# Kernel tuning notes

Measured on AMD Instinct MI355X. Metric: run time of the kernel, lower is better.

The kernel has to match this reference:

```python
import jax, jax.numpy as jnp
import numpy as np

M_FAI = 1024


def _cmul_mm(a, b):
    # complex matmul of (2, M, M) @ (2, M, M) -> (2, M, M)
    re = a[0] @ b[0] - a[1] @ b[1]
    im = a[0] @ b[1] + a[1] @ b[0]
    return jnp.stack([re, im])


def _cmul_el(a, b):
    # elementwise complex multiply, leading dim 2 = (real, imag)
    re = a[0] * b[0] - a[1] * b[1]
    im = a[0] * b[1] + a[1] * b[0]
    return jnp.stack([re, im])


def _diag(x):
    # diagonal of (2, M, M) -> (2, M)
    return jnp.diagonal(x, axis1=1, axis2=2)


def setup_inputs() -> dict:
    key = jax.random.key(0)
    ks = jax.random.split(key, 13)
    mats = {}
    names = ['Theta', 'A1', 'B1', 'C1', 'A2', 'B2', 'C2', 'A3', 'B3', 'C3']
    for i, n in enumerate(names):
        mats[n] = jax.random.normal(ks[i], (2, M_FAI, M_FAI), dtype=jnp.float32)
    mats['alpha'] = jnp.ones((1,), dtype=jnp.float32)
    mats['belta'] = jnp.ones((1,), dtype=jnp.float32)
    # xavier_uniform with gain=0.01 on (2, M_fai): bound = 0.01*sqrt(6/(2+M_fai))
    bound = 0.01 * np.sqrt(6.0 / (2 + M_FAI))
    mats['param1'] = jax.random.uniform(ks[10], (2, M_FAI), dtype=jnp.float32, minval=-bound, maxval=bound)
    mats['param2'] = jax.random.uniform(ks[11], (2, M_FAI), dtype=jnp.float32, minval=-bound, maxval=bound)
    return mats


def reference(Theta, A1, B1, C1, A2, B2, C2, A3, B3, C3, alpha, belta, param1, param2):
    # approximateTheta = cdiag(param1); diag(p) @ C == columnwise complex scale of C rows
    p = param1[:, :, None]  # (2, M, 1)
    Q1 = _cmul_mm(A1, _cmul_el(p, C1))
    Q2 = _cmul_mm(A2, _cmul_el(p, C2))
    Q3 = _cmul_mm(A2, _cmul_el(p, C3))  # original uses A2 here (faithful)

    Thd = _diag(Theta)  # (2, M)
    b1 = alpha * _cmul_el(_diag(A1), _cmul_el(Thd, _diag(C1))) - _diag(Q1) + _diag(B1)
    b2 = belta * _cmul_el(_diag(A2), _cmul_el(Thd, _diag(C2))) - _diag(Q2) + _diag(B2)
    b3 = belta * _cmul_el(_diag(A3), _cmul_el(Thd, _diag(C3))) - _diag(Q3) + _diag(B3)
    b = b1 + b2 + b3 + param2  # (2, M)
    # per-column complex unit-normalize: torch.norm over the (2,1) column
    norm = jnp.sqrt(jnp.sum(b * b, axis=0, keepdims=True))
    theta_new = b / norm  # (2, M)
    # cdiag: embed as (2, M, M) diagonal complex matrix
    Theta_new = jax.vmap(jnp.diag)(theta_new)
    return Theta_new
```

## Files before the change

kernel.cpp:

```cpp
#include <hip/hip_runtime.h>
#include <math.h>

#define M 1024

#define TI 32
#define KCH 32
#define KSPLIT 16
#define KB (M / KSPLIT)

__global__ __launch_bounds__(256)
void diagq_kernel(const float* __restrict__ A1, const float* __restrict__ C1,
                  const float* __restrict__ A2, const float* __restrict__ C2,
                  const float* __restrict__ C3, const float* __restrict__ p1,
                  float* __restrict__ D )
{
    __shared__ float As_re[TI][KCH + 1];
    __shared__ float As_im[TI][KCH + 1];
    __shared__ float Cs_re[KCH][TI];
    __shared__ float Cs_im[KCH][TI];
    __shared__ float red_re[256];
    __shared__ float red_im[256];

    const int t  = threadIdx.x;
    const int i0 = blockIdx.x * TI;
    const int q  = blockIdx.y;
    const int z  = blockIdx.z;
    const int k0 = z * KB;

    const float* __restrict__ A = (q == 0) ? A1 : A2;
    const float* __restrict__ C = (q == 0) ? C1 : ((q == 1) ? C2 : C3);

    const size_t MM = (size_t)M * M;

    const int l_row = t >> 3;
    const int l_c4  = (t & 7) << 2;

    const int i_local = t & 31;
    const int kslice  = t >> 5;

    float acc_re = 0.f, acc_im = 0.f;

    #pragma unroll
    for (int s = 0; s < KB / KCH; ++s) {
        const int kbase = k0 + s * KCH;

        {
            const size_t off = (size_t)(i0 + l_row) * M + kbase + l_c4;
            const float4 are = *(const float4*)(A + off);
            const float4 aim = *(const float4*)(A + MM + off);
            As_re[l_row][l_c4 + 0] = are.x; As_re[l_row][l_c4 + 1] = are.y;
            As_re[l_row][l_c4 + 2] = are.z; As_re[l_row][l_c4 + 3] = are.w;
            As_im[l_row][l_c4 + 0] = aim.x; As_im[l_row][l_c4 + 1] = aim.y;
            As_im[l_row][l_c4 + 2] = aim.z; As_im[l_row][l_c4 + 3] = aim.w;
        }
        {
            const int k = kbase + l_row;
            const float pre = p1[k];
            const float pim = p1[M + k];
            const size_t off = (size_t)k * M + i0 + l_c4;
            const float4 cre = *(const float4*)(C + off);
            const float4 cim = *(const float4*)(C + MM + off);
            Cs_re[l_row][l_c4 + 0] = pre * cre.x - pim * cim.x;
            Cs_re[l_row][l_c4 + 1] = pre * cre.y - pim * cim.y;
            Cs_re[l_row][l_c4 + 2] = pre * cre.z - pim * cim.z;
            Cs_re[l_row][l_c4 + 3] = pre * cre.w - pim * cim.w;
            Cs_im[l_row][l_c4 + 0] = pre * cim.x + pim * cre.x;
            Cs_im[l_row][l_c4 + 1] = pre * cim.y + pim * cre.y;
            Cs_im[l_row][l_c4 + 2] = pre * cim.z + pim * cre.z;
            Cs_im[l_row][l_c4 + 3] = pre * cim.w + pim * cre.w;
        }
        __syncthreads();

        #pragma unroll
        for (int j = 0; j < 4; ++j) {
            const int kk = (kslice << 2) + j;
            const float a_re = As_re[i_local][kk];
            const float a_im = As_im[i_local][kk];
            const float c_re = Cs_re[kk][i_local];
            const float c_im = Cs_im[kk][i_local];
            acc_re += a_re * c_re - a_im * c_im;
            acc_im += a_re * c_im + a_im * c_re;
        }
        __syncthreads();
    }

    red_re[t] = acc_re;
    red_im[t] = acc_im;
    __syncthreads();
    if (t < TI) {
        float sr = 0.f, si = 0.f;
        #pragma unroll
        for (int s = 0; s < 8; ++s) { sr += red_re[t + 32 * s]; si += red_im[t + 32 * s]; }
        D[((size_t)(q * 2 + 0) * KSPLIT + z) * M + i0 + t] = sr;
        D[((size_t)(q * 2 + 1) * KSPLIT + z) * M + i0 + t] = si;
    }
}

__global__ __launch_bounds__(256)
void finalize_kernel(const float* __restrict__ Theta,
                     const float* __restrict__ A1, const float* __restrict__ B1, const float* __restrict__ C1,
                     const float* __restrict__ A2, const float* __restrict__ B2, const float* __restrict__ C2,
                     const float* __restrict__ A3, const float* __restrict__ B3, const float* __restrict__ C3,
                     const float* __restrict__ alpha, const float* __restrict__ belta,
                     const float* __restrict__ p2, const float* __restrict__ D,
                     float* __restrict__ out)
{
    __shared__ float sv[128];

    const int t = threadIdx.x;
    const int i = blockIdx.x;
    const size_t MM = (size_t)M * M;
    const size_t dg = (size_t)i * M + i;

    if (t < 96) {
        sv[t] = D[(size_t)t * M + i];
    } else if (t < 116) {
        const int j = t - 96;
        const float* ptrs[10] = {Theta, A1, B1, C1, A2, B2, C2, A3, B3, C3};
        const float* P = ptrs[j >> 1];
        sv[t] = P[(j & 1) ? (MM + dg) : dg];
    } else if (t == 116) { sv[116] = p2[i]; }
    else if (t == 117)   { sv[117] = p2[M + i]; }
    else if (t == 118)   { sv[118] = alpha[0]; }
    else if (t == 119)   { sv[119] = belta[0]; }

    const float4 z4 = make_float4(0.f, 0.f, 0.f, 0.f);
    ((float4*)(out + (size_t)i * M))[t]      = z4;
    ((float4*)(out + MM + (size_t)i * M))[t] = z4;

    __syncthreads();

    if (t == 0) {
        float qs[6];
        #pragma unroll
        for (int qc = 0; qc < 6; ++qc) {
            float s = 0.f;
            #pragma unroll
            for (int k = 0; k < 16; ++k) s += sv[qc * 16 + k];
            qs[qc] = s;
        }
        const float th_re = sv[96], th_im = sv[97];
        const float al = sv[118], be = sv[119];

        float b_re = sv[116], b_im = sv[117];

        {
            const float a_re = sv[98],  a_im = sv[99];
            const float c_re = sv[102], c_im = sv[103];
            const float t_re = th_re * c_re - th_im * c_im;
            const float t_im = th_re * c_im + th_im * c_re;
            b_re += al * (a_re * t_re - a_im * t_im) - qs[0] + sv[100];
            b_im += al * (a_re * t_im + a_im * t_re) - qs[1] + sv[101];
        }
        {
            const float a_re = sv[104], a_im = sv[105];
            const float c_re = sv[108], c_im = sv[109];
            const float t_re = th_re * c_re - th_im * c_im;
            const float t_im = th_re * c_im + th_im * c_re;
            b_re += be * (a_re * t_re - a_im * t_im) - qs[2] + sv[106];
            b_im += be * (a_re * t_im + a_im * t_re) - qs[3] + sv[107];
        }
        {
            const float a_re = sv[110], a_im = sv[111];
            const float c_re = sv[114], c_im = sv[115];
            const float t_re = th_re * c_re - th_im * c_im;
            const float t_im = th_re * c_im + th_im * c_re;
            b_re += be * (a_re * t_re - a_im * t_im) - qs[4] + sv[112];
            b_im += be * (a_re * t_im + a_im * t_re) - qs[5] + sv[113];
        }

        const float inv = 1.0f / sqrtf(b_re * b_re + b_im * b_im);
        out[dg]      = b_re * inv;
        out[MM + dg] = b_im * inv;
    }
}

extern "C" void kernel_launch(void* const* d_in, const int* in_sizes, int n_in,
                              void* d_out, int out_size, void* d_ws, size_t ws_size,
                              hipStream_t stream) {
    const float* Theta = (const float*)d_in[0];
    const float* A1    = (const float*)d_in[1];
    const float* B1    = (const float*)d_in[2];
    const float* C1    = (const float*)d_in[3];
    const float* A2    = (const float*)d_in[4];
    const float* B2    = (const float*)d_in[5];
    const float* C2    = (const float*)d_in[6];
    const float* A3    = (const float*)d_in[7];
    const float* B3    = (const float*)d_in[8];
    const float* C3    = (const float*)d_in[9];
    const float* alpha = (const float*)d_in[10];
    const float* belta = (const float*)d_in[11];
    const float* p1    = (const float*)d_in[12];
    const float* p2    = (const float*)d_in[13];
    float* out = (float*)d_out;
    float* D   = (float*)d_ws;

    dim3 grid(M / TI, 3, KSPLIT);
    diagq_kernel<<<grid, 256, 0, stream>>>(A1, C1, A2, C2, C3, p1, D);

    finalize_kernel<<<dim3(M), 256, 0, stream>>>(
        Theta, A1, B1, C1, A2, B2, C2, A3, B3, C3, alpha, belta, p2, D, out);
}
```

Baseline: 130.5 us.

## Share A2 tile across Q2/Q3, move output zeroing into diag kernel, thin finalize

The diagonal-Q kernel now runs two block sets instead of three. The second set loads each A2 tile once and accumulates against both C2 and C3, which removes one redundant read pass over A2. Zero-filling the 8 MB output moves from the finalize kernel into the diag kernel, with each block clearing a slice. The finalize kernel becomes one thread per diagonal element and reads its inputs directly, with no shared staging or sync. In exchange, qset blocks carry more shared memory and branch work, and this relies on the zeroing finishing before finalize writes the diagonal, which stream ordering guarantees.

```diff
diff --git a/kernel.cpp b/kernel.cpp
--- a/kernel.cpp
+++ b/kernel.cpp
@@ -12,23 +12,33 @@
 void diagq_kernel(const float* __restrict__ A1, const float* __restrict__ C1,
                   const float* __restrict__ A2, const float* __restrict__ C2,
                   const float* __restrict__ C3, const float* __restrict__ p1,
-                  float* __restrict__ D )
+                  float* __restrict__ D ,
+                  float* __restrict__ out )
 {
     __shared__ float As_re[TI][KCH + 1];
     __shared__ float As_im[TI][KCH + 1];
-    __shared__ float Cs_re[KCH][TI];
-    __shared__ float Cs_im[KCH][TI];
-    __shared__ float red_re[256];
-    __shared__ float red_im[256];
-
-    const int t  = threadIdx.x;
-    const int i0 = blockIdx.x * TI;
-    const int q  = blockIdx.y;
-    const int z  = blockIdx.z;
-    const int k0 = z * KB;
-
-    const float* __restrict__ A = (q == 0) ? A1 : A2;
-    const float* __restrict__ C = (q == 0) ? C1 : ((q == 1) ? C2 : C3);
+    __shared__ float Cb_re[KCH][TI + 1];
+    __shared__ float Cb_im[KCH][TI + 1];
+    __shared__ float Cc_re[KCH][TI + 1];
+    __shared__ float Cc_im[KCH][TI + 1];
+    __shared__ float red[4][256];
+
+    const int t    = threadIdx.x;
+    const int i0   = blockIdx.x * TI;
+    const int qset = blockIdx.y;
+    const int z    = blockIdx.z;
+    const int k0   = z * KB;
+
+    {
+        const int bid = blockIdx.x + 32 * (blockIdx.y + 2 * blockIdx.z);
+        float4* o4 = (float4*)out + (size_t)bid * 512 + t;
+        const float4 z4 = make_float4(0.f, 0.f, 0.f, 0.f);
+        o4[0]   = z4;
+        o4[256] = z4;
+    }
+
+    const float* __restrict__ A  = qset ? A2 : A1;
+    const float* __restrict__ Cb = qset ? C2 : C1;
 
     const size_t MM = (size_t)M * M;
 
@@ -38,7 +48,8 @@
     const int i_local = t & 31;
     const int kslice  = t >> 5;
 
-    float acc_re = 0.f, acc_im = 0.f;
+    float b_re = 0.f, b_im = 0.f;
+    float c_re_acc = 0.f, c_im_acc = 0.f;
 
     #pragma unroll
     for (int s = 0; s < KB / KCH; ++s) {
@@ -53,21 +64,34 @@
             As_im[l_row][l_c4 + 0] = aim.x; As_im[l_row][l_c4 + 1] = aim.y;
             As_im[l_row][l_c4 + 2] = aim.z; As_im[l_row][l_c4 + 3] = aim.w;
         }
+        const int k = kbase + l_row;
+        const float pre = p1[k];
+        const float pim = p1[M + k];
         {
-            const int k = kbase + l_row;
-            const float pre = p1[k];
-            const float pim = p1[M + k];
             const size_t off = (size_t)k * M + i0 + l_c4;
-            const float4 cre = *(const float4*)(C + off);
-            const float4 cim = *(const float4*)(C + MM + off);
-            Cs_re[l_row][l_c4 + 0] = pre * cre.x - pim * cim.x;
-            Cs_re[l_row][l_c4 + 1] = pre * cre.y - pim * cim.y;
-            Cs_re[l_row][l_c4 + 2] = pre * cre.z - pim * cim.z;
-            Cs_re[l_row][l_c4 + 3] = pre * cre.w - pim * cim.w;
-            Cs_im[l_row][l_c4 + 0] = pre * cim.x + pim * cre.x;
-            Cs_im[l_row][l_c4 + 1] = pre * cim.y + pim * cre.y;
-            Cs_im[l_row][l_c4 + 2] = pre * cim.z + pim * cre.z;
-            Cs_im[l_row][l_c4 + 3] = pre * cim.w + pim * cre.w;
+            const float4 cre = *(const float4*)(Cb + off);
+            const float4 cim = *(const float4*)(Cb + MM + off);
+            Cb_re[l_row][l_c4 + 0] = pre * cre.x - pim * cim.x;
+            Cb_re[l_row][l_c4 + 1] = pre * cre.y - pim * cim.y;
+            Cb_re[l_row][l_c4 + 2] = pre * cre.z - pim * cim.z;
+            Cb_re[l_row][l_c4 + 3] = pre * cre.w - pim * cim.w;
+            Cb_im[l_row][l_c4 + 0] = pre * cim.x + pim * cre.x;
+            Cb_im[l_row][l_c4 + 1] = pre * cim.y + pim * cre.y;
+            Cb_im[l_row][l_c4 + 2] = pre * cim.z + pim * cre.z;
+            Cb_im[l_row][l_c4 + 3] = pre * cim.w + pim * cre.w;
+        }
+        if (qset) {
+            const size_t off = (size_t)k * M + i0 + l_c4;
+            const float4 cre = *(const float4*)(C3 + off);
+            const float4 cim = *(const float4*)(C3 + MM + off);
+            Cc_re[l_row][l_c4 + 0] = pre * cre.x - pim * cim.x;
+            Cc_re[l_row][l_c4 + 1] = pre * cre.y - pim * cim.y;
+            Cc_re[l_row][l_c4 + 2] = pre * cre.z - pim * cim.z;
+            Cc_re[l_row][l_c4 + 3] = pre * cre.w - pim * cim.w;
+            Cc_im[l_row][l_c4 + 0] = pre * cim.x + pim * cre.x;
+            Cc_im[l_row][l_c4 + 1] = pre * cim.y + pim * cre.y;
+            Cc_im[l_row][l_c4 + 2] = pre * cim.z + pim * cre.z;
+            Cc_im[l_row][l_c4 + 3] = pre * cim.w + pim * cre.w;
         }
         __syncthreads();
 
@@ -76,27 +100,49 @@
             const int kk = (kslice << 2) + j;
             const float a_re = As_re[i_local][kk];
             const float a_im = As_im[i_local][kk];
-            const float c_re = Cs_re[kk][i_local];
-            const float c_im = Cs_im[kk][i_local];
-            acc_re += a_re * c_re - a_im * c_im;
-            acc_im += a_re * c_im + a_im * c_re;
+            {
+                const float x_re = Cb_re[kk][i_local];
+                const float x_im = Cb_im[kk][i_local];
+                b_re += a_re * x_re - a_im * x_im;
+                b_im += a_re * x_im + a_im * x_re;
+            }
+            if (qset) {
+                const float x_re = Cc_re[kk][i_local];
+                const float x_im = Cc_im[kk][i_local];
+                c_re_acc += a_re * x_re - a_im * x_im;
+                c_im_acc += a_re * x_im + a_im * x_re;
+            }
         }
         __syncthreads();
     }
 
-    red_re[t] = acc_re;
-    red_im[t] = acc_im;
+    red[0][t] = b_re;
+    red[1][t] = b_im;
+    red[2][t] = c_re_acc;
+    red[3][t] = c_im_acc;
     __syncthreads();
     if (t < TI) {
-        float sr = 0.f, si = 0.f;
+        float s0 = 0.f, s1 = 0.f, s2 = 0.f, s3 = 0.f;
         #pragma unroll
-        for (int s = 0; s < 8; ++s) { sr += red_re[t + 32 * s]; si += red_im[t + 32 * s]; }
-        D[((size_t)(q * 2 + 0) * KSPLIT + z) * M + i0 + t] = sr;
-        D[((size_t)(q * 2 + 1) * KSPLIT + z) * M + i0 + t] = si;
+        for (int s = 0; s < 8; ++s) {
+            s0 += red[0][t + 32 * s];
+            s1 += red[1][t + 32 * s];
+            s2 += red[2][t + 32 * s];
+            s3 += red[3][t + 32 * s];
+        }
+        if (qset == 0) {
+            D[((size_t)(0 * KSPLIT) + z) * M + i0 + t] = s0;
+            D[((size_t)(1 * KSPLIT) + z) * M + i0 + t] = s1;
+        } else {
+            D[((size_t)(2 * KSPLIT) + z) * M + i0 + t] = s0;
+            D[((size_t)(3 * KSPLIT) + z) * M + i0 + t] = s1;
+            D[((size_t)(4 * KSPLIT) + z) * M + i0 + t] = s2;
+            D[((size_t)(5 * KSPLIT) + z) * M + i0 + t] = s3;
+        }
     }
 }
 
-__global__ __launch_bounds__(256)
+__global__ __launch_bounds__(128)
 void finalize_kernel(const float* __restrict__ Theta,
                      const float* __restrict__ A1, const float* __restrict__ B1, const float* __restrict__ C1,
                      const float* __restrict__ A2, const float* __restrict__ B2, const float* __restrict__ C2,
@@ -105,74 +151,53 @@
                      const float* __restrict__ p2, const float* __restrict__ D,
                      float* __restrict__ out)
 {
-    __shared__ float sv[128];
-
-    const int t = threadIdx.x;
-    const int i = blockIdx.x;
+    const int i = blockIdx.x * 128 + threadIdx.x;
     const size_t MM = (size_t)M * M;
     const size_t dg = (size_t)i * M + i;
 
-    if (t < 96) {
-        sv[t] = D[(size_t)t * M + i];
-    } else if (t < 116) {
-        const int j = t - 96;
-        const float* ptrs[10] = {Theta, A1, B1, C1, A2, B2, C2, A3, B3, C3};
-        const float* P = ptrs[j >> 1];
-        sv[t] = P[(j & 1) ? (MM + dg) : dg];
-    } else if (t == 116) { sv[116] = p2[i]; }
-    else if (t == 117)   { sv[117] = p2[M + i]; }
-    else if (t == 118)   { sv[118] = alpha[0]; }
-    else if (t == 119)   { sv[119] = belta[0]; }
-
-    const float4 z4 = make_float4(0.f, 0.f, 0.f, 0.f);
-    ((float4*)(out + (size_t)i * M))[t]      = z4;
-    ((float4*)(out + MM + (size_t)i * M))[t] = z4;
-
-    __syncthreads();
-
-    if (t == 0) {
-        float qs[6];
+    float qs[6];
+    #pragma unroll
+    for (int qc = 0; qc < 6; ++qc) {
+        float s = 0.f;
         #pragma unroll
-        for (int qc = 0; qc < 6; ++qc) {
-            float s = 0.f;
-            #pragma unroll
-            for (int k = 0; k < 16; ++k) s += sv[qc * 16 + k];
-            qs[qc] = s;
-        }
-        const float th_re = sv[96], th_im = sv[97];
-        const float al = sv[118], be = sv[119];
-
-        float b_re = sv[116], b_im = sv[117];
-
-        {
-            const float a_re = sv[98],  a_im = sv[99];
-            const float c_re = sv[102], c_im = sv[103];
-            const float t_re = th_re * c_re - th_im * c_im;
-            const float t_im = th_re * c_im + th_im * c_re;
-            b_re += al * (a_re * t_re - a_im * t_im) - qs[0] + sv[100];
-            b_im += al * (a_re * t_im + a_im * t_re) - qs[1] + sv[101];
-        }
-        {
-            const float a_re = sv[104], a_im = sv[105];
-            const float c_re = sv[108], c_im = sv[109];
-            const float t_re = th_re * c_re - th_im * c_im;
-            const float t_im = th_re * c_im + th_im * c_re;
-            b_re += be * (a_re * t_re - a_im * t_im) - qs[2] + sv[106];
-            b_im += be * (a_re * t_im + a_im * t_re) - qs[3] + sv[107];
-        }
-        {
-            const float a_re = sv[110], a_im = sv[111];
-            const float c_re = sv[114], c_im = sv[115];
-            const float t_re = th_re * c_re - th_im * c_im;
-            const float t_im = th_re * c_im + th_im * c_re;
-            b_re += be * (a_re * t_re - a_im * t_im) - qs[4] + sv[112];
-            b_im += be * (a_re * t_im + a_im * t_re) - qs[5] + sv[113];
-        }
-
-        const float inv = 1.0f / sqrtf(b_re * b_re + b_im * b_im);
-        out[dg]      = b_re * inv;
-        out[MM + dg] = b_im * inv;
-    }
+        for (int z = 0; z < KSPLIT; ++z)
+            s += D[((size_t)qc * KSPLIT + z) * M + i];
+        qs[qc] = s;
+    }
+
+    const float th_re = Theta[dg], th_im = Theta[MM + dg];
+    const float al = alpha[0], be = belta[0];
+
+    float b_re = p2[i], b_im = p2[M + i];
+
+    {
+        const float a_re = A1[dg], a_im = A1[MM + dg];
+        const float c_re = C1[dg], c_im = C1[MM + dg];
+        const float t_re = th_re * c_re - th_im * c_im;
+        const float t_im = th_re * c_im + th_im * c_re;
+        b_re += al * (a_re * t_re - a_im * t_im) - qs[0] + B1[dg];
+        b_im += al * (a_re * t_im + a_im * t_re) - qs[1] + B1[MM + dg];
+    }
+    {
+        const float a_re = A2[dg], a_im = A2[MM + dg];
+        const float c_re = C2[dg], c_im = C2[MM + dg];
+        const float t_re = th_re * c_re - th_im * c_im;
+        const float t_im = th_re * c_im + th_im * c_re;
+        b_re += be * (a_re * t_re - a_im * t_im) - qs[2] + B2[dg];
+        b_im += be * (a_re * t_im + a_im * t_re) - qs[3] + B2[MM + dg];
+    }
+    {
+        const float a_re = A3[dg], a_im = A3[MM + dg];
+        const float c_re = C3[dg], c_im = C3[MM + dg];
+        const float t_re = th_re * c_re - th_im * c_im;
+        const float t_im = th_re * c_im + th_im * c_re;
+        b_re += be * (a_re * t_re - a_im * t_im) - qs[4] + B3[dg];
+        b_im += be * (a_re * t_im + a_im * t_re) - qs[5] + B3[MM + dg];
+    }
+
+    const float inv = 1.0f / sqrtf(b_re * b_re + b_im * b_im);
+    out[dg]      = b_re * inv;
+    out[MM + dg] = b_im * inv;
 }
 
 extern "C" void kernel_launch(void* const* d_in, const int* in_sizes, int n_in,
@@ -195,9 +220,9 @@
     float* out = (float*)d_out;
     float* D   = (float*)d_ws;
 
-    dim3 grid(M / TI, 3, KSPLIT);
-    diagq_kernel<<<grid, 256, 0, stream>>>(A1, C1, A2, C2, C3, p1, D);
-
-    finalize_kernel<<<dim3(M), 256, 0, stream>>>(
+    dim3 grid(M / TI, 2, KSPLIT);
+    diagq_kernel<<<grid, 256, 0, stream>>>(A1, C1, A2, C2, C3, p1, D, out);
+
+    finalize_kernel<<<dim3(M / 128), 128, 0, stream>>>(
         Theta, A1, B1, C1, A2, B2, C2, A3, B3, C3, alpha, belta, p2, D, out);
 }
```

After: 129.4 us. No clear change (-0.9%).
